# Performance work log

Measured on AMD Instinct MI355X. Metric: run time of the kernel, lower is better.

Reference implementation:

```python
import jax, jax.numpy as jnp
import numpy as np

NEG = -9.0e15


def setup_inputs() -> dict:
    key = jax.random.key(0)
    k_x, k_w, k_e, k_b, k_m = jax.random.split(key, 5)
    B, N, C, F = 2048, 64, 256, 256
    x = jax.random.normal(k_x, (B, N, C), dtype=jnp.float32)
    W = jax.random.normal(k_w, (2, C, F), dtype=jnp.float32) * (1.414 / np.sqrt(C + F))
    # full logit tensor; only entries where mask holds are ever read (equivalent
    # to torch's flat `e` scattered into the nonzero positions of adj)
    e = jax.random.normal(k_e, (F, N, N), dtype=jnp.float32)
    bias = jax.random.normal(k_b, (F,), dtype=jnp.float32) * (1.0 / np.sqrt(C))
    # symmetric adjacency mask with self-loops, density ~0.3
    m = jax.random.bernoulli(k_m, 0.3, (N, N))
    mask = (m | m.T) | jnp.eye(N, dtype=bool)
    return {"x": x, "W": W, "e": e, "bias": bias, "mask": mask}


def reference(x, W, e, bias, mask):
    # x: [B,N,C], W: [2,C,F], e: [F,N,N], bias: [F], mask: [N,N] bool
    h0 = x @ W[0]                                   # [B,N,F] (self term)
    h1 = x @ W[1]                                   # [B,N,F] (neighbor term)
    logits = jnp.where(mask[None, :, :], e, NEG)    # [F,N,N]
    adj = jax.nn.softmax(logits, axis=2)            # per-channel row softmax
    N = mask.shape[0]
    eye = jnp.eye(N, dtype=bool)
    d = jnp.diagonal(adj, axis1=1, axis2=2)         # [F,N]  (adj * E diagonal)
    off = jnp.where(eye[None, :, :], 0.0, adj)      # [F,N,N] (adj * (1-E))
    # (adj*E) @ h0 reduces to per-node diagonal scaling; off-diag is a
    # per-channel NxN matmul batched over B.
    out = d.T[None, :, :] * h0 + jnp.einsum('fnm,bmf->bnf', off, h1)
    return out + bias[None, None, :]
```

## Files before the change

kernel.cpp:

```cpp
#include <hip/hip_runtime.h>
#include <hip/hip_bf16.h>


typedef __attribute__((ext_vector_type(8))) short  fragA;
typedef __attribute__((ext_vector_type(4))) float  f32x4;
typedef __attribute__((ext_vector_type(8))) unsigned short u16x8;
typedef __attribute__((ext_vector_type(4))) unsigned short u16x4;

constexpr long OFF_OFF = 0;
constexpr long OFF_WT  = 2l * 1024 * 1024;
constexpr long OFF_DS  = OFF_WT + 512l * 256 * 2;
constexpr long OFF_XB  = OFF_DS + 64l * 256 * 4;
constexpr long OFF_G0  = OFF_XB + 131072l * 256 * 2;
constexpr long OFF_H1T = OFF_G0 + 131072l * 256 * 2;
constexpr long WS_NEED = OFF_H1T + 131072l * 256 * 2;

static __device__ inline unsigned short f2bf(float f) {
  __hip_bfloat16 h = __float2bfloat16(f);
  return __builtin_bit_cast(unsigned short, h);
}
static __device__ inline float bf2f(unsigned short u) {
  unsigned int x = ((unsigned int)u) << 16;
  return __builtin_bit_cast(float, x);
}
static __device__ __forceinline__ void gl16(const void* g, void* l) {
  __builtin_amdgcn_global_load_lds(
      (const __attribute__((address_space(1))) unsigned int*)g,
      (__attribute__((address_space(3))) unsigned int*)l, 16, 0, 0);
}
static __device__ __forceinline__ f32x4 mfma16(fragA a, fragA b, f32x4 c) {
  return __builtin_amdgcn_mfma_f32_16x16x32_bf16(a, b, c, 0, 0, 0);
}

__global__ __launch_bounds__(256) void k_pre(const float* __restrict__ x,
                                             const float* __restrict__ e,
                                             const float* __restrict__ W,
                                             const unsigned char* __restrict__ mask,
                                             char* __restrict__ ws_b) {
  const int bid = blockIdx.x;
  const int tid = threadIdx.x;
  if (bid < 4096) {
    unsigned short* off = (unsigned short*)(ws_b + OFF_OFF);
    float* dscale = (float*)(ws_b + OFF_DS);
    const int lane = tid & 63;
    const int row  = bid * 4 + (tid >> 6);
    const int n = row & 63;
    bool is_u8 = __all(mask[lane * 65] != 0);
    bool mv;
    if (is_u8) mv = mask[n * 64 + lane] != 0;
    else       mv = ((const int*)mask)[n * 64 + lane] != 0;
    float v = mv ? e[(long)row * 64 + lane] : -1e30f;
    float mx = v;
#pragma unroll
    for (int s = 32; s; s >>= 1) mx = fmaxf(mx, __shfl_xor(mx, s));
    float ex = mv ? __expf(v - mx) : 0.f;
    float sm = ex;
#pragma unroll
    for (int s = 32; s; s >>= 1) sm += __shfl_xor(sm, s);
    float adj = ex / sm;
    const int f = row >> 6;
    if (lane == n) dscale[n * 256 + f] = adj;
    off[(long)row * 64 + lane] = f2bf(lane == n ? 0.f : adj);
  } else if (bid < 6144) {
    unsigned short* xb = (unsigned short*)(ws_b + OFF_XB);
    long i = ((long)(bid - 4096) * 256 + tid) * 8;
    const long stride = 2048l * 256 * 8;
    const long total = 131072l * 256;
    for (; i < total; i += stride) {
      float4 a = *(const float4*)(x + i);
      float4 b = *(const float4*)(x + i + 4);
      u16x8 p;
      p[0] = f2bf(a.x); p[1] = f2bf(a.y); p[2] = f2bf(a.z); p[3] = f2bf(a.w);
      p[4] = f2bf(b.x); p[5] = f2bf(b.y); p[6] = f2bf(b.z); p[7] = f2bf(b.w);
      *(u16x8*)(xb + i) = p;
    }
  } else {
    unsigned short* Wt = (unsigned short*)(ws_b + OFF_WT);
    __shared__ float t[64][65];
    const int b2 = bid - 6144;
    const int w = b2 >> 4, f0 = ((b2 >> 2) & 3) * 64, c0 = (b2 & 3) * 64;
    const int tr = tid >> 2, tc = (tid & 3) * 16;
    const float* src = W + ((long)(w * 256 + c0 + tr)) * 256 + f0 + tc;
#pragma unroll
    for (int i = 0; i < 16; i += 4) {
      float4 v = *(const float4*)(src + i);
      t[tr][tc + i] = v.x; t[tr][tc + i + 1] = v.y;
      t[tr][tc + i + 2] = v.z; t[tr][tc + i + 3] = v.w;
    }
    __syncthreads();
    u16x8 p0, p1;
#pragma unroll
    for (int i = 0; i < 8; i++)  p0[i] = f2bf(t[tc + i][tr]);
#pragma unroll
    for (int i = 0; i < 8; i++)  p1[i] = f2bf(t[tc + 8 + i][tr]);
    unsigned short* dst = Wt + ((long)(w * 256 + f0 + tr)) * 256 + c0 + tc;
    *(u16x8*)dst = p0;
    *(u16x8*)(dst + 8) = p1;
  }
}

__global__ __launch_bounds__(256, 5) void k_gemm(char* __restrict__ ws_b) {
  const float* dscale = (const float*)(ws_b + OFF_DS);
  const char* xb_b = ws_b + OFF_XB;
  const char* wt_b = ws_b + OFF_WT;
  unsigned short* g0g = (unsigned short*)(ws_b + OFF_G0);
  unsigned short* h1t = (unsigned short*)(ws_b + OFF_H1T);

  __shared__ __align__(16) char arena[24576];

  const int tid = threadIdx.x;
  const int wid = tid >> 6, lane = tid & 63;
  const int lr = lane & 15, qu = lane >> 4;

  const int wg = blockIdx.x;
  const int xcd = wg & 7, s = wg >> 3;
  const int rg = xcd * 128 + (s >> 3);
  const int cg = s & 7;
  const int f0 = cg * 32;
  const long R0 = (long)rg * 128;

  const int ar   = tid >> 3;
  const int aswz = (((tid & 7) ^ (ar & 7)) << 4);
  const int wrow0 = f0 + ar;
  const int wrow1 = 256 + f0 + ar;

  auto STAGE = [&](int ks) {
    const long ko = (long)ks * 128;
#pragma unroll
    for (int i = 0; i < 4; i++)
      gl16(xb_b + (R0 + i * 32 + ar) * 512 + ko + aswz,
           arena + i * 4096 + tid * 16);
    gl16(wt_b + (long)wrow0 * 512 + ko + aswz, arena + 16384 + tid * 16);
    gl16(wt_b + (long)wrow1 * 512 + ko + aswz, arena + 16384 + 4096 + tid * 16);
  };

  STAGE(0);
  f32x4 acc[2][4] = {};
  const int arow0 = wid * 32;

  for (int ks = 0; ks < 4; ks++) {
    __syncthreads();
#pragma unroll
    for (int kk = 0; kk < 2; kk++) {
      fragA af[2], bfr[4];
#pragma unroll
      for (int i2 = 0; i2 < 2; i2++) {
        int r = arow0 + i2 * 16 + lr;
        af[i2] = *(const fragA*)(arena + r * 128 +
                     ((kk * 64 + qu * 16) ^ ((lr & 7) << 4)));
      }
#pragma unroll
      for (int j = 0; j < 4; j++) {
        int cc = j * 16 + lr;
        bfr[j] = *(const fragA*)(arena + 16384 + cc * 128 +
                     ((kk * 64 + qu * 16) ^ ((lr & 7) << 4)));
      }
#pragma unroll
      for (int i2 = 0; i2 < 2; i2++)
#pragma unroll
        for (int j = 0; j < 4; j++)
          acc[i2][j] = mfma16(af[i2], bfr[j], acc[i2][j]);
    }
    __syncthreads();
    if (ks < 3) STAGE(ks + 1);
  }

  unsigned short* Gs = (unsigned short*)(arena);
  unsigned short* Ts = (unsigned short*)(arena + 10240);
#pragma unroll
  for (int i2 = 0; i2 < 2; i2++) {
#pragma unroll
    for (int j = 0; j < 2; j++) {
      int f = f0 + j * 16 + lr;
#pragma unroll
      for (int r = 0; r < 4; r++) {
        int rloc = arow0 + i2 * 16 + qu * 4 + r;
        int n = rloc & 63;
        Gs[rloc * 40 + j * 16 + lr] = f2bf(dscale[n * 256 + f] * acc[i2][j][r]);
      }
    }
#pragma unroll
    for (int j = 2; j < 4; j++) {
      int fl = (j - 2) * 16 + lr;
      int rb = arow0 + i2 * 16 + qu * 4;
      u16x4 pk;
      pk[0] = f2bf(acc[i2][j][0]); pk[1] = f2bf(acc[i2][j][1]);
      pk[2] = f2bf(acc[i2][j][2]); pk[3] = f2bf(acc[i2][j][3]);
      *(u16x4*)(Ts + fl * 136 + rb) = pk;
    }
  }
  __syncthreads();

  {
    int row = tid >> 1, half = tid & 1;
    const unsigned short* sp = Gs + row * 40 + half * 16;
    unsigned short* dp = g0g + (R0 + row) * 256 + f0 + half * 16;
    *(u16x8*)dp = *(const u16x8*)sp;
    *(u16x8*)(dp + 8) = *(const u16x8*)(sp + 8);
  }
  {
    int f = tid >> 3, seg = tid & 7;
    const unsigned short* sp = Ts + f * 136 + seg * 16;
    unsigned short* dp = h1t + (long)(f0 + f) * 131072 + R0 + seg * 16;
    *(u16x8*)dp = *(const u16x8*)sp;
    *(u16x8*)(dp + 8) = *(const u16x8*)(sp + 8);
  }
}

__global__ __launch_bounds__(256, 4) void k_eout(const float* __restrict__ bias,
                                                 const char* __restrict__ ws_b,
                                                 float* __restrict__ out) {
  const unsigned short* offp = (const unsigned short*)(ws_b + OFF_OFF);
  const unsigned short* h1t  = (const unsigned short*)(ws_b + OFF_H1T);
  const unsigned short* g0g  = (const unsigned short*)(ws_b + OFF_G0);

  __shared__ __align__(16) unsigned short Es[16 * 1088];

  const int tid = threadIdx.x;
  const int wid = tid >> 6, lane = tid & 63;
  const int lr = lane & 15, qu = lane >> 4;

  const int wg = blockIdx.x;
  const int xcd = wg & 7, u = wg >> 3;
  const int bg = xcd * 16 + (u >> 4);
  const int fg = u & 15;
  const long B0 = (long)bg * 16;
  const int f0 = fg * 16;

  fragA hb0[4], hb1[4];
#pragma unroll
  for (int q = 0; q < 4; q++) {
    const unsigned short* hp =
        h1t + (long)(f0 + wid * 4 + q) * 131072 + (B0 + lr) * 64 + qu * 8;
    hb0[q] = *(const fragA*)hp;
    hb1[q] = *(const fragA*)(hp + 32);
  }

#pragma unroll
  for (int q = 0; q < 4; q++) {
    const int fi = wid * 4 + q;
    const unsigned short* ob = offp + (long)(f0 + fi) * 4096;
    f32x4 ea[4] = {};
#pragma unroll
    for (int ct = 0; ct < 4; ct++) {
      fragA o0 = *(const fragA*)(ob + (ct * 16 + lr) * 64 + qu * 8);
      fragA o1 = *(const fragA*)(ob + (ct * 16 + lr) * 64 + 32 + qu * 8);
      ea[ct] = mfma16(o0, hb0[q], ea[ct]);
      ea[ct] = mfma16(o1, hb1[q], ea[ct]);
    }
#pragma unroll
    for (int ct = 0; ct < 4; ct++) {
      u16x4 pk;
      pk[0] = f2bf(ea[ct][0]); pk[1] = f2bf(ea[ct][1]);
      pk[2] = f2bf(ea[ct][2]); pk[3] = f2bf(ea[ct][3]);
      *(u16x4*)&Es[fi * 1088 + lr * 68 + ct * 16 + qu * 4] = pk;
    }
  }

  u16x8 gv[4][2];
#pragma unroll
  for (int i = 0; i < 4; i++) {
    int rl = tid + 256 * i;
    int b = rl >> 6, n = rl & 63;
    const unsigned short* gp = g0g + ((B0 + b) * 64 + n) * 256 + f0;
    gv[i][0] = ((const u16x8*)gp)[0];
    gv[i][1] = ((const u16x8*)gp)[1];
  }
  float4 bv[4];
#pragma unroll
  for (int k = 0; k < 4; k++) bv[k] = ((const float4*)(bias + f0))[k];

  __syncthreads();

#pragma unroll
  for (int i = 0; i < 4; i++) {
    int rl = tid + 256 * i;
    int b = rl >> 6, n = rl & 63;
    float es[16];
#pragma unroll
    for (int k = 0; k < 16; k++)
      es[k] = bf2f(Es[k * 1088 + b * 68 + n]);
    float4* op = (float4*)(out + ((B0 + b) * 64 + n) * 256 + f0);
#pragma unroll
    for (int k = 0; k < 4; k++) {
      float4 ov;
      ov.x = bf2f(gv[i][k >> 1][(k & 1) * 4 + 0]) + es[k * 4 + 0] + bv[k].x;
      ov.y = bf2f(gv[i][k >> 1][(k & 1) * 4 + 1]) + es[k * 4 + 1] + bv[k].y;
      ov.z = bf2f(gv[i][k >> 1][(k & 1) * 4 + 2]) + es[k * 4 + 2] + bv[k].z;
      ov.w = bf2f(gv[i][k >> 1][(k & 1) * 4 + 3]) + es[k * 4 + 3] + bv[k].w;
      op[k] = ov;
    }
  }
}

extern "C" void kernel_launch(void* const* d_in, const int* in_sizes, int n_in,
                              void* d_out, int out_size, void* d_ws, size_t ws_size,
                              hipStream_t stream) {
  const float* x    = (const float*)d_in[0];
  const float* W    = (const float*)d_in[1];
  const float* e    = (const float*)d_in[2];
  const float* bias = (const float*)d_in[3];
  const unsigned char* mask = (const unsigned char*)d_in[4];
  float* out = (float*)d_out;
  char* ws = (char*)d_ws;
  if (ws_size < (size_t)WS_NEED) return;

  k_pre<<<6176, 256, 0, stream>>>(x, e, W, mask, ws);
  k_gemm<<<8192, 256, 0, stream>>>(ws);
  k_eout<<<2048, 256, 0, stream>>>(bias, ws, out);
}
```

Before: 216.7 us.

## Remap k_eout waves over node tiles to drop LDS transpose and barrier

The epilogue kernel now gives each wave a 16-node slice across all 16 channels instead of 4 channels across all nodes. The MFMA results stay in registers as packed bf16 pairs and are written straight to the output, with no shared-memory staging and no __syncthreads. This also raises the launch-bounds occupancy hint from 4 to 5 blocks per SM. In exchange, each thread's output stores are now strided by row, so each store covers fewer contiguous bytes, which may hurt write coalescing.

```diff
diff --git a/kernel.cpp b/kernel.cpp
--- a/kernel.cpp
+++ b/kernel.cpp
@@ -22,6 +22,9 @@
 static __device__ inline float bf2f(unsigned short u) {
   unsigned int x = ((unsigned int)u) << 16;
   return __builtin_bit_cast(float, x);
+}
+static __device__ inline unsigned int packbf(float a, float b) {
+  return (unsigned int)f2bf(a) | ((unsigned int)f2bf(b) << 16);
 }
 static __device__ __forceinline__ void gl16(const void* g, void* l) {
   __builtin_amdgcn_global_load_lds(
@@ -207,14 +210,12 @@
   }
 }
 
-__global__ __launch_bounds__(256, 4) void k_eout(const float* __restrict__ bias,
+__global__ __launch_bounds__(256, 5) void k_eout(const float* __restrict__ bias,
                                                  const char* __restrict__ ws_b,
                                                  float* __restrict__ out) {
   const unsigned short* offp = (const unsigned short*)(ws_b + OFF_OFF);
   const unsigned short* h1t  = (const unsigned short*)(ws_b + OFF_H1T);
   const unsigned short* g0g  = (const unsigned short*)(ws_b + OFF_G0);
-
-  __shared__ __align__(16) unsigned short Es[16 * 1088];
 
   const int tid = threadIdx.x;
   const int wid = tid >> 6, lane = tid & 63;
@@ -226,68 +227,60 @@
   const int fg = u & 15;
   const long B0 = (long)bg * 16;
   const int f0 = fg * 16;
-
-  fragA hb0[4], hb1[4];
-#pragma unroll
-  for (int q = 0; q < 4; q++) {
-    const unsigned short* hp =
-        h1t + (long)(f0 + wid * 4 + q) * 131072 + (B0 + lr) * 64 + qu * 8;
-    hb0[q] = *(const fragA*)hp;
-    hb1[q] = *(const fragA*)(hp + 32);
-  }
-
-#pragma unroll
-  for (int q = 0; q < 4; q++) {
-    const int fi = wid * 4 + q;
-    const unsigned short* ob = offp + (long)(f0 + fi) * 4096;
-    f32x4 ea[4] = {};
-#pragma unroll
-    for (int ct = 0; ct < 4; ct++) {
-      fragA o0 = *(const fragA*)(ob + (ct * 16 + lr) * 64 + qu * 8);
-      fragA o1 = *(const fragA*)(ob + (ct * 16 + lr) * 64 + 32 + qu * 8);
-      ea[ct] = mfma16(o0, hb0[q], ea[ct]);
-      ea[ct] = mfma16(o1, hb1[q], ea[ct]);
-    }
-#pragma unroll
-    for (int ct = 0; ct < 4; ct++) {
-      u16x4 pk;
-      pk[0] = f2bf(ea[ct][0]); pk[1] = f2bf(ea[ct][1]);
-      pk[2] = f2bf(ea[ct][2]); pk[3] = f2bf(ea[ct][3]);
-      *(u16x4*)&Es[fi * 1088 + lr * 68 + ct * 16 + qu * 4] = pk;
-    }
-  }
-
-  u16x8 gv[4][2];
-#pragma unroll
-  for (int i = 0; i < 4; i++) {
-    int rl = tid + 256 * i;
-    int b = rl >> 6, n = rl & 63;
-    const unsigned short* gp = g0g + ((B0 + b) * 64 + n) * 256 + f0;
-    gv[i][0] = ((const u16x8*)gp)[0];
-    gv[i][1] = ((const u16x8*)gp)[1];
-  }
+  const int nw = wid * 16;
+
+  const unsigned short* obase = offp + (long)f0 * 4096 + (nw + lr) * 64 + qu * 8;
+  const unsigned short* hbase = h1t + (long)f0 * 131072 + (B0 + lr) * 64 + qu * 8;
+
+  unsigned int eb[4][8];
+
+#pragma unroll
+  for (int fp = 0; fp < 8; fp++) {
+    const unsigned short* ob0 = obase + (long)(2 * fp) * 4096;
+    const unsigned short* hb0 = hbase + (long)(2 * fp) * 131072;
+    const unsigned short* ob1 = ob0 + 4096;
+    const unsigned short* hb1 = hb0 + 131072;
+    fragA oa0 = *(const fragA*)(ob0);
+    fragA oa1 = *(const fragA*)(ob0 + 32);
+    fragA ha0 = *(const fragA*)(hb0);
+    fragA ha1 = *(const fragA*)(hb0 + 32);
+    fragA oc0 = *(const fragA*)(ob1);
+    fragA oc1 = *(const fragA*)(ob1 + 32);
+    fragA hc0 = *(const fragA*)(hb1);
+    fragA hc1 = *(const fragA*)(hb1 + 32);
+    f32x4 e0 = {}, e1 = {};
+    e0 = mfma16(oa0, ha0, e0);
+    e1 = mfma16(oc0, hc0, e1);
+    e0 = mfma16(oa1, ha1, e0);
+    e1 = mfma16(oc1, hc1, e1);
+#pragma unroll
+    for (int j = 0; j < 4; j++)
+      eb[j][fp] = packbf(e0[j], e1[j]);
+  }
+
   float4 bv[4];
 #pragma unroll
   for (int k = 0; k < 4; k++) bv[k] = ((const float4*)(bias + f0))[k];
 
-  __syncthreads();
-
-#pragma unroll
-  for (int i = 0; i < 4; i++) {
-    int rl = tid + 256 * i;
-    int b = rl >> 6, n = rl & 63;
-    float es[16];
-#pragma unroll
-    for (int k = 0; k < 16; k++)
-      es[k] = bf2f(Es[k * 1088 + b * 68 + n]);
-    float4* op = (float4*)(out + ((B0 + b) * 64 + n) * 256 + f0);
+#pragma unroll
+  for (int j = 0; j < 4; j++) {
+    long R = (B0 + lr) * 64 + nw + qu * 4 + j;
+    const unsigned short* gp = g0g + R * 256 + f0;
+    u16x8 gv0 = ((const u16x8*)gp)[0];
+    u16x8 gv1 = ((const u16x8*)gp)[1];
+    float4* op = (float4*)(out + R * 256 + f0);
 #pragma unroll
     for (int k = 0; k < 4; k++) {
+      unsigned int p0 = eb[j][k * 2], p1 = eb[j][k * 2 + 1];
+      float g0e = bf2f(k < 2 ? gv0[k * 4 + 0] : gv1[(k - 2) * 4 + 0]);
+      float g1e = bf2f(k < 2 ? gv0[k * 4 + 1] : gv1[(k - 2) * 4 + 1]);
+      float g2e = bf2f(k < 2 ? gv0[k * 4 + 2] : gv1[(k - 2) * 4 + 2]);
+      float g3e = bf2f(k < 2 ? gv0[k * 4 + 3] : gv1[(k - 2) * 4 + 3]);
       float4 ov;
-      ov.x = bf2f(gv[i][k >> 1][(k & 1) * 4 + 0]) + es[k * 4 + 0] + bv[k].x;
-      ov.y = bf2f(gv[i][k >> 1][(k & 1) * 4 + 1]) + es[k * 4 + 1] + bv[k].y;
-      ov.z = bf2f(gv[i][k >> 1][(k & 1) * 4 + 2]) + es[k * 4 + 2] + bv[k].z;
-      ov.w = bf2f(gv[i][k >> 1][(k & 1) * 4 + 3]) + es[k * 4 + 3] + bv[k].w;
+      ov.x = g0e + bf2f((unsigned short)(p0 & 0xffff)) + bv[k].x;
+      ov.y = g1e + bf2f((unsigned short)(p0 >> 16)) + bv[k].y;
+      ov.z = g2e + bf2f((unsigned short)(p1 & 0xffff)) + bv[k].z;
+      ov.w = g3e + bf2f((unsigned short)(p1 >> 16)) + bv[k].w;
       op[k] = ov;
     }
   }
```

Result: slower. 241.6 us (+11.5%).
